# Kernel optimization log

Measured on AMD Instinct MI355X. Metric: run time of the kernel, lower is better.

Reference implementation:

```python
import jax, jax.numpy as jnp
import numpy as np

N, IN_C, OUT_C = 8192, 256, 256


def setup_inputs() -> dict:
    key = jax.random.key(0)
    ks = jax.random.split(key, 12)
    p = lambda k, shape: (jax.random.normal(k, shape, jnp.float32) * 0.05)
    return {
        "X": jax.random.normal(ks[0], (IN_C,), jnp.float32),
        "head": 100,
        "tail": 7,
        "E": jax.random.uniform(ks[1], (N, N), jnp.float32),
        "H": jax.random.normal(ks[2], (N, OUT_C), jnp.float32),
        "W_x_z": p(ks[3], (IN_C, OUT_C)),
        "W_h_z": p(ks[4], (OUT_C, OUT_C)),
        "conv_z": p(ks[5], (OUT_C, OUT_C)),
        "b_z": jnp.zeros((1, OUT_C), jnp.float32),
        "W_x_r": p(ks[6], (IN_C, OUT_C)),
        "W_h_r": p(ks[7], (OUT_C, OUT_C)),
        "conv_r": p(ks[8], (OUT_C, OUT_C)),
        "b_r": jnp.zeros((1, OUT_C), jnp.float32),
        "W_x_h": p(ks[9], (IN_C, OUT_C)),
        "W_h_h": p(ks[10], (OUT_C, OUT_C)),
        "b_h": jnp.zeros((1, OUT_C), jnp.float32),
    }


def reference(X, head, tail, E, H, W_x_z, W_h_z, conv_z, b_z,
              W_x_r, W_h_r, conv_r, b_r, W_x_h, W_h_h, b_h):
    # --- edge-weight update ---
    # Original: M = 0.5*I with M[head,tail]=0.5; Ep = E with Ep[head,tail]+=1;
    # E_new = M @ Ep.  M@Ep scales every row by 0.5 and (if head!=tail) adds
    # 0.5*Ep[tail] into row `head`.  Same math, O(N^2) instead of O(N^3).
    Ep = E.at[head, tail].add(1.0)
    E_new = 0.5 * Ep
    if head != tail:  # head/tail are Python ints (static)
        E_new = E_new.at[head].add(0.5 * Ep[tail])

    h_head = H[head]                 # [OUT_C]
    agg = E_new[head] @ H            # GCN aggregation over neighbors: [OUT_C]

    Z = jax.nn.sigmoid(X @ W_x_z + h_head @ W_h_z + agg @ conv_z + b_z[0])
    R = jax.nn.sigmoid(X @ W_x_r + h_head @ W_h_r + agg @ conv_r + b_r[0])
    H_tilde = jnp.tanh(X @ W_x_h + (h_head * R) @ W_h_h + b_h[0])

    H_new = H.at[head].set(Z * h_head + (1.0 - Z) * H_tilde)
    return E_new, H_new
```

## Files before the change

### kernel.cpp

```cpp
#include <hip/hip_runtime.h>
#include <math.h>

#define NN 8192
#define CC 256
#define LOG2N 13

typedef float f32x4 __attribute__((ext_vector_type(4)));

#define WS_AGGP 0
#define WS_ZRP  32768

__global__ void __launch_bounds__(256) k_agg(
        const float* __restrict__ E, const float* __restrict__ H,
        const int* __restrict__ dh, const int* __restrict__ dt,
        float* __restrict__ aggP) {
    __shared__ float e_sh[64];
    __shared__ f32x4 red[4][64];
    const int head = dh[0], tail = dt[0];
    const int t = threadIdx.x;
    const int i0 = blockIdx.x * 64;
    if (t < 64) {
        const int i = i0 + t;
        float e = 0.5f * E[(size_t)head * NN + i];
        if (head != tail) e += 0.5f * E[(size_t)tail * NN + i];
        if (i == tail) e += 0.5f;
        e_sh[t] = e;
    }
    __syncthreads();
    const int g = t >> 6, c = (t & 63) << 2;
    f32x4 acc = {0.f, 0.f, 0.f, 0.f};
    #pragma unroll
    for (int it = 0; it < 16; ++it) {
        const int r = it * 4 + g;
        const f32x4 hv = *(const f32x4*)(H + (size_t)(i0 + r) * CC + c);
        acc += hv * e_sh[r];
    }
    red[g][t & 63] = acc;
    __syncthreads();
    if (g == 0) {
        const f32x4 s = red[0][t] + red[1][t] + red[2][t] + red[3][t];
        *(f32x4*)(aggP + blockIdx.x * CC + (t << 2)) = s;
    }
}

__global__ void __launch_bounds__(256) k_mv(
        const float* __restrict__ X, const float* __restrict__ H,
        const int* __restrict__ dh,
        const float* __restrict__ Wxz, const float* __restrict__ Whz,
        const float* __restrict__ Cz,  const float* __restrict__ Wxr,
        const float* __restrict__ Whr, const float* __restrict__ Cr,
        const float* __restrict__ Wxh,
        const float* __restrict__ aggP, float* __restrict__ zrP) {
    __shared__ float v_sh[64];
    const int m = blockIdx.x >> 2, q = blockIdx.x & 3;
    const int t = threadIdx.x;
    const float* W;
    switch (m) {
        case 0: W = Wxz; break; case 1: W = Whz; break; case 2: W = Cz; break;
        case 3: W = Wxr; break; case 4: W = Whr; break; case 5: W = Cr; break;
        default: W = Wxh; break;
    }
    if (t < 64) {
        const int k = q * 64 + t;
        float v;
        if (m == 1 || m == 4)      v = H[(size_t)dh[0] * CC + k];
        else if (m == 2 || m == 5) { v = 0.f; for (int b = 0; b < 128; ++b) v += aggP[b * CC + k]; }
        else                       v = X[k];
        v_sh[t] = v;
    }
    __syncthreads();
    float acc = 0.f;
    #pragma unroll
    for (int kk = 0; kk < 64; ++kk)
        acc += v_sh[kk] * W[(size_t)(q * 64 + kk) * CC + t];
    zrP[(m * 4 + q) * CC + t] = acc;
}

__global__ void __launch_bounds__(256) k_big(
        const float* __restrict__ E, const float* __restrict__ H,
        const int* __restrict__ dh, const int* __restrict__ dt,
        const float* __restrict__ bz, const float* __restrict__ br,
        const float* __restrict__ bh, const float* __restrict__ Whh,
        const float* __restrict__ zrP, float* __restrict__ out) {
    const int head = dh[0], tail = dt[0];
    const size_t nn = (size_t)NN * NN;

    if (blockIdx.x == 0) {
        __shared__ float rs_sh[CC];
        const int c = threadIdx.x;
        float sz = bz[c], sr = br[c];
        #pragma unroll
        for (int p = 0; p < 12; ++p)  sz += zrP[p * CC + c];
        #pragma unroll
        for (int p = 12; p < 24; ++p) sr += zrP[p * CC + c];
        const float z = 1.f / (1.f + expf(-sz));
        const float r = 1.f / (1.f + expf(-sr));
        const float h = H[(size_t)head * CC + c];
        rs_sh[c] = h * r;
        __syncthreads();
        float acc = 0.f;
        #pragma unroll 16
        for (int k = 0; k < CC; ++k)
            acc += rs_sh[k] * Whh[(size_t)k * CC + c];
        float s = bh[c] + acc;
        #pragma unroll
        for (int p = 24; p < 28; ++p) s += zrP[p * CC + c];
        const float ht = tanhf(s);
        out[nn + (size_t)head * CC + c] = z * h + (1.f - z) * ht;
        return;
    }

    const size_t total4 = (nn + (size_t)NN * CC) >> 2;
    const size_t nstream = (size_t)(gridDim.x - 1) * blockDim.x;
    for (size_t idx = (size_t)(blockIdx.x - 1) * blockDim.x + threadIdx.x;
         idx < total4; idx += nstream) {
        const size_t e = idx << 2;
        if (e < nn) {
            const f32x4 v = __builtin_nontemporal_load((const f32x4*)(E + e));
            f32x4 o = v * 0.5f;
            const int i = (int)(e >> LOG2N);
            if (i == head) {
                const int j = (int)(e & (NN - 1));
                if (head != tail) {
                    const f32x4 w = *(const f32x4*)(E + (size_t)tail * NN + j);
                    o += w * 0.5f;
                }
                if (tail >= j && tail < j + 4) o[tail - j] += 0.5f;
            }
            __builtin_nontemporal_store(o, (f32x4*)(out + e));
        } else {
            const size_t tt = e - nn;
            if ((int)(tt >> 8) != head) {
                const f32x4 hv = __builtin_nontemporal_load((const f32x4*)(H + tt));
                __builtin_nontemporal_store(hv, (f32x4*)(out + nn + tt));
            }
        }
    }
}

extern "C" void kernel_launch(void* const* d_in, const int* in_sizes, int n_in,
                              void* d_out, int out_size, void* d_ws, size_t ws_size,
                              hipStream_t stream) {
    const float* X    = (const float*)d_in[0];
    const int*   dh   = (const int*)d_in[1];
    const int*   dt   = (const int*)d_in[2];
    const float* E    = (const float*)d_in[3];
    const float* H    = (const float*)d_in[4];
    const float* Wxz  = (const float*)d_in[5];
    const float* Whz  = (const float*)d_in[6];
    const float* Cz   = (const float*)d_in[7];
    const float* bz   = (const float*)d_in[8];
    const float* Wxr  = (const float*)d_in[9];
    const float* Whr  = (const float*)d_in[10];
    const float* Cr   = (const float*)d_in[11];
    const float* br   = (const float*)d_in[12];
    const float* Wxh  = (const float*)d_in[13];
    const float* Whh  = (const float*)d_in[14];
    const float* bh   = (const float*)d_in[15];
    float* out = (float*)d_out;
    float* ws  = (float*)d_ws;

    float* aggP = ws + WS_AGGP;
    float* zrP  = ws + WS_ZRP;

    k_agg<<<128, 256, 0, stream>>>(E, H, dh, dt, aggP);
    k_mv<<<28, 256, 0, stream>>>(X, H, dh, Wxz, Whz, Cz, Wxr, Whr, Cr, Wxh, aggP, zrP);
    k_big<<<2049, 256, 0, stream>>>(E, H, dh, dt, bz, br, bh, Whh, zrP, out);
}
```

Before: 114.1 us.

## Fuse agg, matvec and streaming kernels into one launch with atomic counters

Merges the three kernels into a single launch where block ranges take different roles: aggregation blocks (which now also copy H to the output), matvec blocks that spin-wait on a counter for the aggregation partials, an epilogue block that waits for all matvecs, and streaming blocks that scale E. This removes two kernel launch gaps and lets the small GRU work overlap the bandwidth-bound E stream. E stores switch from nontemporal to regular stores, and each streaming block now handles a fixed contiguous chunk. It adds a memset launch and relies on the low-numbered dependency blocks being scheduled before waiting blocks, so a different dispatch order could deadlock.

```diff
diff --git a/kernel.cpp b/kernel.cpp
--- a/kernel.cpp
+++ b/kernel.cpp
@@ -9,85 +9,141 @@
 
 #define WS_AGGP 0
 #define WS_ZRP  32768
+#define WS_CNT  39936
 
-__global__ void __launch_bounds__(256) k_agg(
-        const float* __restrict__ E, const float* __restrict__ H,
+#define NAGG    128
+#define NMV     28
+#define BID_EPI (NAGG + NMV)
+#define STREAM0 (BID_EPI + 1)
+#define NSTREAM 2048
+
+__global__ void __launch_bounds__(256) k_fused(
+        const float* __restrict__ X, const float* __restrict__ E,
+        const float* __restrict__ H,
         const int* __restrict__ dh, const int* __restrict__ dt,
-        float* __restrict__ aggP) {
-    __shared__ float e_sh[64];
-    __shared__ f32x4 red[4][64];
-    const int head = dh[0], tail = dt[0];
-    const int t = threadIdx.x;
-    const int i0 = blockIdx.x * 64;
-    if (t < 64) {
-        const int i = i0 + t;
-        float e = 0.5f * E[(size_t)head * NN + i];
-        if (head != tail) e += 0.5f * E[(size_t)tail * NN + i];
-        if (i == tail) e += 0.5f;
-        e_sh[t] = e;
-    }
-    __syncthreads();
-    const int g = t >> 6, c = (t & 63) << 2;
-    f32x4 acc = {0.f, 0.f, 0.f, 0.f};
-    #pragma unroll
-    for (int it = 0; it < 16; ++it) {
-        const int r = it * 4 + g;
-        const f32x4 hv = *(const f32x4*)(H + (size_t)(i0 + r) * CC + c);
-        acc += hv * e_sh[r];
-    }
-    red[g][t & 63] = acc;
-    __syncthreads();
-    if (g == 0) {
-        const f32x4 s = red[0][t] + red[1][t] + red[2][t] + red[3][t];
-        *(f32x4*)(aggP + blockIdx.x * CC + (t << 2)) = s;
-    }
-}
-
-__global__ void __launch_bounds__(256) k_mv(
-        const float* __restrict__ X, const float* __restrict__ H,
-        const int* __restrict__ dh,
         const float* __restrict__ Wxz, const float* __restrict__ Whz,
         const float* __restrict__ Cz,  const float* __restrict__ Wxr,
         const float* __restrict__ Whr, const float* __restrict__ Cr,
-        const float* __restrict__ Wxh,
-        const float* __restrict__ aggP, float* __restrict__ zrP) {
-    __shared__ float v_sh[64];
-    const int m = blockIdx.x >> 2, q = blockIdx.x & 3;
+        const float* __restrict__ Wxh, const float* __restrict__ Whh,
+        const float* __restrict__ bz, const float* __restrict__ br,
+        const float* __restrict__ bh,
+        float* __restrict__ ws, unsigned* __restrict__ cnt,
+        float* __restrict__ out) {
+    const int bid = blockIdx.x;
     const int t = threadIdx.x;
-    const float* W;
-    switch (m) {
-        case 0: W = Wxz; break; case 1: W = Whz; break; case 2: W = Cz; break;
-        case 3: W = Wxr; break; case 4: W = Whr; break; case 5: W = Cr; break;
-        default: W = Wxh; break;
-    }
-    if (t < 64) {
-        const int k = q * 64 + t;
-        float v;
-        if (m == 1 || m == 4)      v = H[(size_t)dh[0] * CC + k];
-        else if (m == 2 || m == 5) { v = 0.f; for (int b = 0; b < 128; ++b) v += aggP[b * CC + k]; }
-        else                       v = X[k];
-        v_sh[t] = v;
-    }
-    __syncthreads();
-    float acc = 0.f;
-    #pragma unroll
-    for (int kk = 0; kk < 64; ++kk)
-        acc += v_sh[kk] * W[(size_t)(q * 64 + kk) * CC + t];
-    zrP[(m * 4 + q) * CC + t] = acc;
-}
-
-__global__ void __launch_bounds__(256) k_big(
-        const float* __restrict__ E, const float* __restrict__ H,
-        const int* __restrict__ dh, const int* __restrict__ dt,
-        const float* __restrict__ bz, const float* __restrict__ br,
-        const float* __restrict__ bh, const float* __restrict__ Whh,
-        const float* __restrict__ zrP, float* __restrict__ out) {
     const int head = dh[0], tail = dt[0];
     const size_t nn = (size_t)NN * NN;
+    float* aggP = ws + WS_AGGP;
+    float* zrP  = ws + WS_ZRP;
 
-    if (blockIdx.x == 0) {
+    if (bid >= STREAM0) {
+        const int s = bid - STREAM0;
+        const size_t base = (size_t)s * 8192 + t;
+        #pragma unroll 4
+        for (int k = 0; k < 32; ++k) {
+            const size_t idx = base + (size_t)k * 256;
+            const size_t e = idx << 2;
+            const f32x4 v = __builtin_nontemporal_load((const f32x4*)(E + e));
+            f32x4 o = v * 0.5f;
+            const int i = (int)(e >> LOG2N);
+            if (i == head) {
+                const int j = (int)(e & (NN - 1));
+                if (head != tail) {
+                    const f32x4 w = *(const f32x4*)(E + (size_t)tail * NN + j);
+                    o += w * 0.5f;
+                }
+                if (tail >= j && tail < j + 4) o[tail - j] += 0.5f;
+            }
+            *(f32x4*)(out + e) = o;
+        }
+        return;
+    }
+
+    if (bid < NAGG) {
+        __shared__ float e_sh[64];
+        __shared__ f32x4 red[4][64];
+        const int i0 = bid * 64;
+        if (t < 64) {
+            const int i = i0 + t;
+            float e = 0.5f * E[(size_t)head * NN + i];
+            if (head != tail) e += 0.5f * E[(size_t)tail * NN + i];
+            if (i == tail) e += 0.5f;
+            e_sh[t] = e;
+        }
+        __syncthreads();
+        const int g = t >> 6, c = (t & 63) << 2;
+        f32x4 acc = {0.f, 0.f, 0.f, 0.f};
+        #pragma unroll
+        for (int it = 0; it < 16; ++it) {
+            const int r = it * 4 + g;
+            const int row = i0 + r;
+            const f32x4 hv = __builtin_nontemporal_load(
+                (const f32x4*)(H + (size_t)row * CC + c));
+            acc += hv * e_sh[r];
+            if (row != head)
+                *(f32x4*)(out + nn + (size_t)row * CC + c) = hv;
+        }
+        red[g][t & 63] = acc;
+        __syncthreads();
+        if (g == 0) {
+            const f32x4 sv = red[0][t] + red[1][t] + red[2][t] + red[3][t];
+            *(f32x4*)(aggP + bid * CC + (t << 2)) = sv;
+        }
+        __threadfence();
+        __syncthreads();
+        if (t == 0)
+            __hip_atomic_fetch_add(&cnt[0], 1u, __ATOMIC_RELEASE, __HIP_MEMORY_SCOPE_AGENT);
+        return;
+    }
+
+    if (bid < BID_EPI) {
+        const int mb = bid - NAGG;
+        const int m = mb >> 2, q = mb & 3;
+        __shared__ float v_sh[64];
+        const float* W;
+        switch (m) {
+            case 0: W = Wxz; break; case 1: W = Whz; break; case 2: W = Cz; break;
+            case 3: W = Wxr; break; case 4: W = Whr; break; case 5: W = Cr; break;
+            default: W = Wxh; break;
+        }
+        if (m == 2 || m == 5) {
+            if (t == 0) {
+                while (__hip_atomic_load(&cnt[0], __ATOMIC_ACQUIRE,
+                                         __HIP_MEMORY_SCOPE_AGENT) < NAGG)
+                    __builtin_amdgcn_s_sleep(1);
+            }
+            __syncthreads();
+        }
+        if (t < 64) {
+            const int k = q * 64 + t;
+            float v;
+            if (m == 1 || m == 4)      v = H[(size_t)head * CC + k];
+            else if (m == 2 || m == 5) { v = 0.f; for (int b = 0; b < NAGG; ++b) v += aggP[b * CC + k]; }
+            else                       v = X[k];
+            v_sh[t] = v;
+        }
+        __syncthreads();
+        float acc = 0.f;
+        #pragma unroll
+        for (int kk = 0; kk < 64; ++kk)
+            acc += v_sh[kk] * W[(size_t)(q * 64 + kk) * CC + t];
+        zrP[mb * CC + t] = acc;
+        __threadfence();
+        __syncthreads();
+        if (t == 0)
+            __hip_atomic_fetch_add(&cnt[1], 1u, __ATOMIC_RELEASE, __HIP_MEMORY_SCOPE_AGENT);
+        return;
+    }
+
+    {
+        if (t == 0) {
+            while (__hip_atomic_load(&cnt[1], __ATOMIC_ACQUIRE,
+                                     __HIP_MEMORY_SCOPE_AGENT) < NMV)
+                __builtin_amdgcn_s_sleep(1);
+        }
+        __syncthreads();
         __shared__ float rs_sh[CC];
-        const int c = threadIdx.x;
+        const int c = t;
         float sz = bz[c], sr = br[c];
         #pragma unroll
         for (int p = 0; p < 12; ++p)  sz += zrP[p * CC + c];
@@ -107,34 +163,6 @@
         for (int p = 24; p < 28; ++p) s += zrP[p * CC + c];
         const float ht = tanhf(s);
         out[nn + (size_t)head * CC + c] = z * h + (1.f - z) * ht;
-        return;
-    }
-
-    const size_t total4 = (nn + (size_t)NN * CC) >> 2;
-    const size_t nstream = (size_t)(gridDim.x - 1) * blockDim.x;
-    for (size_t idx = (size_t)(blockIdx.x - 1) * blockDim.x + threadIdx.x;
-         idx < total4; idx += nstream) {
-        const size_t e = idx << 2;
-        if (e < nn) {
-            const f32x4 v = __builtin_nontemporal_load((const f32x4*)(E + e));
-            f32x4 o = v * 0.5f;
-            const int i = (int)(e >> LOG2N);
-            if (i == head) {
-                const int j = (int)(e & (NN - 1));
-                if (head != tail) {
-                    const f32x4 w = *(const f32x4*)(E + (size_t)tail * NN + j);
-                    o += w * 0.5f;
-                }
-                if (tail >= j && tail < j + 4) o[tail - j] += 0.5f;
-            }
-            __builtin_nontemporal_store(o, (f32x4*)(out + e));
-        } else {
-            const size_t tt = e - nn;
-            if ((int)(tt >> 8) != head) {
-                const f32x4 hv = __builtin_nontemporal_load((const f32x4*)(H + tt));
-                __builtin_nontemporal_store(hv, (f32x4*)(out + nn + tt));
-            }
-        }
     }
 }
 
@@ -159,11 +187,10 @@
     const float* bh   = (const float*)d_in[15];
     float* out = (float*)d_out;
     float* ws  = (float*)d_ws;
+    unsigned* cnt = (unsigned*)(ws + WS_CNT);
 
-    float* aggP = ws + WS_AGGP;
-    float* zrP  = ws + WS_ZRP;
-
-    k_agg<<<128, 256, 0, stream>>>(E, H, dh, dt, aggP);
-    k_mv<<<28, 256, 0, stream>>>(X, H, dh, Wxz, Whz, Cz, Wxr, Whr, Cr, Wxh, aggP, zrP);
-    k_big<<<2049, 256, 0, stream>>>(E, H, dh, dt, bz, br, bh, Whh, zrP, out);
+    hipMemsetAsync(cnt, 0, 2 * sizeof(unsigned), stream);
+    k_fused<<<STREAM0 + NSTREAM, 256, 0, stream>>>(
+        X, E, H, dh, dt, Wxz, Whz, Cz, Wxr, Whr, Cr, Wxh, Whh,
+        bz, br, bh, ws, cnt, out);
 }
```

After: 148.1 us. 29.8% more time.

## Fuse H copy into aggregation kernel and unroll E streaming loop

Applied to the files above, without the earlier changes.

The aggregation kernel already reads all of H, so it now writes each non-head H row to the output while it has it, which removes the separate H copy pass from the big streaming kernel. The E scaling loop becomes a fixed 8x4 unrolled pattern that issues four independent nontemporal loads before processing, giving more memory-level parallelism. The output stores also switch from nontemporal to regular stores. The hardcoded trip count assumes a grid of exactly 2048 streaming blocks, and the H copy now runs on only 128 blocks.

```diff
diff --git a/kernel.cpp b/kernel.cpp
--- a/kernel.cpp
+++ b/kernel.cpp
@@ -13,12 +13,13 @@
 __global__ void __launch_bounds__(256) k_agg(
         const float* __restrict__ E, const float* __restrict__ H,
         const int* __restrict__ dh, const int* __restrict__ dt,
-        float* __restrict__ aggP) {
+        float* __restrict__ aggP, float* __restrict__ out) {
     __shared__ float e_sh[64];
     __shared__ f32x4 red[4][64];
     const int head = dh[0], tail = dt[0];
     const int t = threadIdx.x;
     const int i0 = blockIdx.x * 64;
+    const size_t nn = (size_t)NN * NN;
     if (t < 64) {
         const int i = i0 + t;
         float e = 0.5f * E[(size_t)head * NN + i];
@@ -32,8 +33,11 @@
     #pragma unroll
     for (int it = 0; it < 16; ++it) {
         const int r = it * 4 + g;
-        const f32x4 hv = *(const f32x4*)(H + (size_t)(i0 + r) * CC + c);
+        const int row = i0 + r;
+        const f32x4 hv = *(const f32x4*)(H + (size_t)row * CC + c);
         acc += hv * e_sh[r];
+        if (row != head)
+            *(f32x4*)(out + nn + (size_t)row * CC + c) = hv;
     }
     red[g][t & 63] = acc;
     __syncthreads();
@@ -110,31 +114,31 @@
         return;
     }
 
-    const size_t total4 = (nn + (size_t)NN * CC) >> 2;
-    const size_t nstream = (size_t)(gridDim.x - 1) * blockDim.x;
-    for (size_t idx = (size_t)(blockIdx.x - 1) * blockDim.x + threadIdx.x;
-         idx < total4; idx += nstream) {
-        const size_t e = idx << 2;
-        if (e < nn) {
-            const f32x4 v = __builtin_nontemporal_load((const f32x4*)(E + e));
-            f32x4 o = v * 0.5f;
+    const size_t step = (size_t)2048 * 256;
+    size_t idx = (size_t)(blockIdx.x - 1) * 256 + threadIdx.x;
+
+    #pragma unroll
+    for (int grp = 0; grp < 8; ++grp) {
+        f32x4 v[4];
+        #pragma unroll
+        for (int j = 0; j < 4; ++j)
+            v[j] = __builtin_nontemporal_load((const f32x4*)(E + ((idx + (size_t)j * step) << 2)));
+        #pragma unroll
+        for (int j = 0; j < 4; ++j) {
+            const size_t e = (idx + (size_t)j * step) << 2;
+            f32x4 o = v[j] * 0.5f;
             const int i = (int)(e >> LOG2N);
             if (i == head) {
-                const int j = (int)(e & (NN - 1));
+                const int jj = (int)(e & (NN - 1));
                 if (head != tail) {
-                    const f32x4 w = *(const f32x4*)(E + (size_t)tail * NN + j);
+                    const f32x4 w = *(const f32x4*)(E + (size_t)tail * NN + jj);
                     o += w * 0.5f;
                 }
-                if (tail >= j && tail < j + 4) o[tail - j] += 0.5f;
+                if (tail >= jj && tail < jj + 4) o[tail - jj] += 0.5f;
             }
-            __builtin_nontemporal_store(o, (f32x4*)(out + e));
-        } else {
-            const size_t tt = e - nn;
-            if ((int)(tt >> 8) != head) {
-                const f32x4 hv = __builtin_nontemporal_load((const f32x4*)(H + tt));
-                __builtin_nontemporal_store(hv, (f32x4*)(out + nn + tt));
-            }
+            *(f32x4*)(out + e) = o;
         }
+        idx += 4 * step;
     }
 }
 
@@ -163,7 +167,7 @@
     float* aggP = ws + WS_AGGP;
     float* zrP  = ws + WS_ZRP;
 
-    k_agg<<<128, 256, 0, stream>>>(E, H, dh, dt, aggP);
+    k_agg<<<128, 256, 0, stream>>>(E, H, dh, dt, aggP, out);
     k_mv<<<28, 256, 0, stream>>>(X, H, dh, Wxz, Whz, Cz, Wxr, Whr, Cr, Wxh, aggP, zrP);
     k_big<<<2049, 256, 0, stream>>>(E, H, dh, dt, bz, br, bh, Whh, zrP, out);
 }
```

New measurement: 120.0 us. 1.05x slower.
